# Optimization experiments

Measured on AMD Instinct MI355X. Metric: run time of the kernel, lower is better.

## Reference

```python
import jax, jax.numpy as jnp
import numpy as np
from jax import lax

EMBED = 512
HID = 512
CLASSES = 3
TP, TH, B = 256, 256, 128
IN_DIM = 768


def _gru_cell(x, h, Wih, Whh, bih, bhh):
    # PyTorch GRU cell math. x: [B, in], h: [B, d]
    gi = x @ Wih.T + bih
    gh = h @ Whh.T + bhh
    i_r, i_z, i_n = jnp.split(gi, 3, axis=-1)
    h_r, h_z, h_n = jnp.split(gh, 3, axis=-1)
    r = jax.nn.sigmoid(i_r + h_r)
    z = jax.nn.sigmoid(i_z + h_z)
    n = jnp.tanh(i_n + r * h_n)
    return (1.0 - z) * n + z * h


def _gru_scan(x, h0, Wih, Whh, bih, bhh):
    # x: [T, B, in]; returns outputs [T, B, d]
    def step(h, xt):
        h = _gru_cell(xt, h, Wih, Whh, bih, bhh)
        return h, h
    _, o = lax.scan(step, h0, x)
    return o


def setup_inputs() -> dict:
    key = jax.random.key(0)
    ks = jax.random.split(key, 32)
    s = 0.02
    d = {
        'encoded_p': jax.random.normal(ks[0], (TP, B, IN_DIM), jnp.float32),
        'encoded_h': jax.random.normal(ks[1], (TH, B, IN_DIM), jnp.float32),
        'p_W': jax.random.normal(ks[2], (EMBED, IN_DIM), jnp.float32) * s,
        'p_b': jnp.zeros((EMBED,), jnp.float32),
        'h_W': jax.random.normal(ks[3], (EMBED, IN_DIM), jnp.float32) * s,
        'h_b': jnp.zeros((EMBED,), jnp.float32),
        'pg_Wih': jax.random.normal(ks[4], (3 * HID, EMBED), jnp.float32) * s,
        'pg_Whh': jax.random.normal(ks[5], (3 * HID, HID), jnp.float32) * s,
        'pg_bih': jnp.zeros((3 * HID,), jnp.float32),
        'pg_bhh': jnp.zeros((3 * HID,), jnp.float32),
        'hg_Wih': jax.random.normal(ks[6], (3 * HID, EMBED), jnp.float32) * s,
        'hg_Whh': jax.random.normal(ks[7], (3 * HID, HID), jnp.float32) * s,
        'hg_bih': jnp.zeros((3 * HID,), jnp.float32),
        'hg_bhh': jnp.zeros((3 * HID,), jnp.float32),
        'W_s': jax.random.normal(ks[8], (HID, HID), jnp.float32) * s,
        'W_t': jax.random.normal(ks[9], (HID, HID), jnp.float32) * s,
        'w_e': jax.random.normal(ks[10], (HID, 1), jnp.float32) * s,
        'W_m': jax.random.normal(ks[11], (HID, HID), jnp.float32) * s,
        'm_Wih': jax.random.normal(ks[12], (3 * HID, 2 * HID), jnp.float32) * s,
        'm_Whh': jax.random.normal(ks[13], (3 * HID, HID), jnp.float32) * s,
        'm_bih': jnp.zeros((3 * HID,), jnp.float32),
        'm_bhh': jnp.zeros((3 * HID,), jnp.float32),
        'out_W': jax.random.normal(ks[14], (CLASSES, HID), jnp.float32) * s,
        'out_b': jnp.zeros((CLASSES,), jnp.float32),
        'training': 0,
    }
    return d


def reference(encoded_p, encoded_h, p_W, p_b, h_W, h_b,
              pg_Wih, pg_Whh, pg_bih, pg_bhh,
              hg_Wih, hg_Whh, hg_bih, hg_bhh,
              W_s, W_t, w_e, W_m,
              m_Wih, m_Whh, m_bih, m_bhh,
              out_W, out_b, training):
    batch = encoded_p.shape[1]
    # dropout is identity when training is falsy (reference uses training=0)
    xp = encoded_p @ p_W.T + p_b          # [Tp, B, embed]
    xh = encoded_h @ h_W.T + h_b          # [Th, B, embed]
    h0 = jnp.ones((batch, HID), xp.dtype)  # torch.ones init hidden
    o_p = _gru_scan(xp, h0, pg_Wih, pg_Whh, pg_bih, pg_bhh)  # [Tp, B, d]
    o_h = _gru_scan(xh, h0, hg_Wih, hg_Whh, hg_bih, hg_bhh)  # [Th, B, d]

    Whs = jnp.einsum('tbd,de->tbe', o_p, W_s)  # precompute, fixed across steps
    we = w_e[:, 0]

    def step(h_m, h_t):
        Wht = h_t @ W_t                        # [B, d]
        Wm = h_m @ W_m                         # [B, d]
        M = jnp.tanh(Whs + (Wht + Wm)[None])   # [Tp, B, d]
        logits = jnp.einsum('tbd,d->bt', M, we)  # [B, Tp]
        alpha = jax.nn.softmax(logits, axis=1)
        a_t = jnp.einsum('bt,tbd->bd', alpha, o_p)
        m_t = jnp.concatenate([a_t, h_t], axis=-1)  # [B, 2d]
        h_m = _gru_cell(m_t, h_m, m_Wih, m_Whh, m_bih, m_bhh)
        return h_m, alpha

    h_m0 = jnp.ones((batch, HID), xp.dtype)
    h_star, _alphas = lax.scan(step, h_m0, o_h)
    out = h_star @ out_W.T + out_b
    out = jax.nn.relu(out)  # LAST_NON_LINEAR = True
    return out
```

## Files before the change

kernel.cpp:

```cpp
#include <hip/hip_runtime.h>
#include <cstddef>

#define TSEQ 256
#define NB   128
#define HID  512
#define G3   1536
#define INDIM 768
#define CH   16
#define NWG  256
#define FLS  32

typedef unsigned short bfraw;
using short8 = __attribute__((ext_vector_type(8))) short;
using f32x4  = __attribute__((ext_vector_type(4))) float;

#define MFMA16 __builtin_amdgcn_mfma_f32_16x16x32_bf16

__device__ __forceinline__ float bf2f(unsigned int u){ return __uint_as_float(u<<16); }
__device__ __forceinline__ bfraw f2bf(float f){
  unsigned int u = __float_as_uint(f);
  u += 0x7fffu + ((u>>16)&1u);
  return (bfraw)(u>>16);
}
__device__ __forceinline__ float fsig(float x){
  return __builtin_amdgcn_rcpf(1.0f + __expf(-x));
}
__device__ __forceinline__ float ftanh(float x){
  return 1.0f - 2.0f*__builtin_amdgcn_rcpf(1.0f + __expf(2.0f*x));
}
__device__ __forceinline__ float4 bpf4(const void* p){
  unsigned long long a = __hip_atomic_load((const unsigned long long*)p,     __ATOMIC_RELAXED, __HIP_MEMORY_SCOPE_AGENT);
  unsigned long long b = __hip_atomic_load((const unsigned long long*)p + 1, __ATOMIC_RELAXED, __HIP_MEMORY_SCOPE_AGENT);
  union{ unsigned long long q[2]; float4 f; } cv; cv.q[0]=a; cv.q[1]=b; return cv.f;
}

__device__ __forceinline__ void spin_ge(unsigned* p, unsigned epoch){
  int sp = 0;
  while (__hip_atomic_load(p, __ATOMIC_RELAXED, __HIP_MEMORY_SCOPE_AGENT) < epoch){
    if (sp < 3){ __builtin_amdgcn_s_sleep(1); ++sp; }
    else        __builtin_amdgcn_s_sleep(16);
  }
}

__device__ __forceinline__ void pollN(unsigned* flags, int n, unsigned epoch){
  const int tid = threadIdx.x;
  if (tid < n) spin_ge(&flags[tid*FLS], epoch);
  __syncthreads();
  if (tid == 0)
    (void)__hip_atomic_load(&flags[0], __ATOMIC_ACQUIRE, __HIP_MEMORY_SCOPE_AGENT);
  __syncthreads();
}
__device__ __forceinline__ void setflag(unsigned* f, unsigned v){
  if (threadIdx.x == 0)
    __hip_atomic_store(f, v, __ATOMIC_RELEASE, __HIP_MEMORY_SCOPE_AGENT);
}

__global__ void init_k(unsigned* bar){
  int i = blockIdx.x*256 + threadIdx.x;
  if (i < 4*NWG*FLS) bar[i] = 0u;
}

__global__ void hminit_k(float* hmbuf, bfraw* hm_bf){
  int i = blockIdx.x*256 + threadIdx.x;
  hmbuf[i] = 1.0f;
  hm_bf[i] = (bfraw)0x3f80;
}

__global__ __launch_bounds__(256)
void tconv_k(const float* __restrict__ in, bfraw* __restrict__ out, int R, int Cc){
  __shared__ float t[32][33];
  int c0 = blockIdx.x*32, r0 = blockIdx.y*32;
  int tx = threadIdx.x&31, ty = threadIdx.x>>5;
  #pragma unroll
  for (int i=0;i<32;i+=8) t[ty+i][tx] = in[(size_t)(r0+ty+i)*Cc + c0+tx];
  __syncthreads();
  #pragma unroll
  for (int i=0;i<32;i+=8) out[(size_t)(c0+ty+i)*R + r0+tx] = f2bf(t[tx][ty+i]);
}

__global__ void cvt_k(const float* __restrict__ in, bfraw* __restrict__ out, int n){
  int i = (blockIdx.x*256 + threadIdx.x)*4;
  if (i >= n) return;
  float4 v = *(const float4*)(in+i);
  uint2 o;
  o.x = (unsigned)f2bf(v.x) | ((unsigned)f2bf(v.y)<<16);
  o.y = (unsigned)f2bf(v.z) | ((unsigned)f2bf(v.w)<<16);
  *(uint2*)(out+i) = o;
}

__global__ void wcat_k(const float* __restrict__ mWih, const float* __restrict__ mWhh,
                       bfraw* __restrict__ Wcat){
  size_t gid = (size_t)blockIdx.x*256 + threadIdx.x;
  int np = (int)(gid / 384);
  int k4 = ((int)(gid % 384))*4;
  int dd = np>>2, g = np&3;
  float v[4];
  #pragma unroll
  for (int j=0;j<4;++j){
    int k = k4+j; float x = 0.f;
    if (g==0)      x = (k<1024) ? mWih[(size_t)dd*1024 + k]        : mWhh[(size_t)dd*512 + (k-1024)];
    else if (g==1) x = (k<1024) ? mWih[(size_t)(512+dd)*1024 + k]  : mWhh[(size_t)(512+dd)*512 + (k-1024)];
    else if (g==2) x = (k<1024) ? mWih[(size_t)(1024+dd)*1024 + k] : 0.f;
    else           x = (k<1024) ? 0.f : mWhh[(size_t)(1024+dd)*512 + (k-1024)];
    v[j] = x;
  }
  uint2 o;
  o.x = (unsigned)f2bf(v[0]) | ((unsigned)f2bf(v[1])<<16);
  o.y = (unsigned)f2bf(v[2]) | ((unsigned)f2bf(v[3])<<16);
  *(uint2*)(Wcat + (size_t)np*1536 + k4) = o;
}

__global__ void bpack_k(const float* __restrict__ mbih, const float* __restrict__ mbhh,
                        float* __restrict__ bc){
  int dd = blockIdx.x*256 + threadIdx.x;
  if (dd >= 512) return;
  bc[dd]      = mbih[dd] + mbhh[dd];
  bc[512+dd]  = mbih[512+dd] + mbhh[512+dd];
  bc[1024+dd] = mbih[1024+dd];
  bc[1536+dd] = mbhh[1024+dd];
}

__global__ void fuse_bias_k(const float* __restrict__ Wih, const float* __restrict__ bih,
                            const float* __restrict__ pb, float* __restrict__ bout)
{
  int g = blockIdx.x*256 + threadIdx.x;
  if (g >= G3) return;
  float acc = bih[g];
  const float* w = Wih + (size_t)g*HID;
  for (int e=0;e<HID;e+=4){
    float4 wv = *(const float4*)(w+e);
    float4 pv = *(const float4*)(pb+e);
    acc += wv.x*pv.x + wv.y*pv.y + wv.z*pv.z + wv.w*pv.w;
  }
  bout[g] = acc;
}

template<typename TA, typename TC, bool BIAS>
__global__ __launch_bounds__(256)
void mgemm(const TA* __restrict__ A0, const TA* __restrict__ A1,
           const bfraw* __restrict__ B0, const bfraw* __restrict__ B1,
           const float* __restrict__ bias0, const float* __restrict__ bias1,
           TC* __restrict__ C0, TC* __restrict__ C1,
           int K, int lda, int ldb, int ldc)
{
  const TA* A = blockIdx.z ? A1 : A0;
  const bfraw* B = blockIdx.z ? B1 : B0;
  const float* bias = blockIdx.z ? bias1 : bias0;
  TC* C = blockIdx.z ? C1 : C0;
  __shared__ bfraw Al[128*40];
  __shared__ bfraw Bl[128*40];
  const int tid = threadIdx.x;
  const size_t m0 = (size_t)blockIdx.y*128, n0 = (size_t)blockIdx.x*128;
  const int w = tid>>6, l = tid&63;
  const int wr = (w>>1)*64, wc = (w&1)*64;
  const int fr = l&15, fg = l>>4;
  f32x4 acc[4][4];
  #pragma unroll
  for (int i=0;i<4;++i)
    #pragma unroll
    for (int j=0;j<4;++j) acc[i][j] = (f32x4){0.f,0.f,0.f,0.f};

  const int srow = tid>>1, skc = (tid&1)*16;
  for (int k0=0; k0<K; k0+=32){
    if constexpr (sizeof(TA)==4){
      const float* ap = (const float*)A + (m0+srow)*lda + k0 + skc;
      float4 v0=*(const float4*)ap, v1=*(const float4*)(ap+4),
             v2=*(const float4*)(ap+8), v3=*(const float4*)(ap+12);
      uint4 w0, w1;
      w0.x=(unsigned)f2bf(v0.x)|((unsigned)f2bf(v0.y)<<16);
      w0.y=(unsigned)f2bf(v0.z)|((unsigned)f2bf(v0.w)<<16);
      w0.z=(unsigned)f2bf(v1.x)|((unsigned)f2bf(v1.y)<<16);
      w0.w=(unsigned)f2bf(v1.z)|((unsigned)f2bf(v1.w)<<16);
      w1.x=(unsigned)f2bf(v2.x)|((unsigned)f2bf(v2.y)<<16);
      w1.y=(unsigned)f2bf(v2.z)|((unsigned)f2bf(v2.w)<<16);
      w1.z=(unsigned)f2bf(v3.x)|((unsigned)f2bf(v3.y)<<16);
      w1.w=(unsigned)f2bf(v3.z)|((unsigned)f2bf(v3.w)<<16);
      *(uint4*)&Al[srow*40+skc]   = w0;
      *(uint4*)&Al[srow*40+skc+8] = w1;
    } else {
      const bfraw* ap = (const bfraw*)A + (m0+srow)*lda + k0 + skc;
      *(uint4*)&Al[srow*40+skc]   = *(const uint4*)ap;
      *(uint4*)&Al[srow*40+skc+8] = *(const uint4*)(ap+8);
    }
    {
      const bfraw* bp = B + (n0+srow)*ldb + k0 + skc;
      *(uint4*)&Bl[srow*40+skc]   = *(const uint4*)bp;
      *(uint4*)&Bl[srow*40+skc+8] = *(const uint4*)(bp+8);
    }
    __syncthreads();
    short8 af[4], bfr[4];
    #pragma unroll
    for (int i=0;i<4;++i) af[i]  = *(const short8*)&Al[(wr+i*16+fr)*40 + fg*8];
    #pragma unroll
    for (int j=0;j<4;++j) bfr[j] = *(const short8*)&Bl[(wc+j*16+fr)*40 + fg*8];
    #pragma unroll
    for (int i=0;i<4;++i)
      #pragma unroll
      for (int j=0;j<4;++j)
        acc[i][j] = MFMA16(af[i], bfr[j], acc[i][j], 0,0,0);
    __syncthreads();
  }
  #pragma unroll
  for (int i=0;i<4;++i){
    #pragma unroll
    for (int j=0;j<4;++j){
      size_t n = n0 + wc + j*16 + fr;
      float bv = BIAS ? bias[n] : 0.f;
      #pragma unroll
      for (int r=0;r<4;++r){
        size_t m = m0 + wr + i*16 + fg*4 + r;
        float v = acc[i][j][r] + bv;
        if constexpr (sizeof(TC)==2) ((bfraw*)C)[m*ldc + n] = f2bf(v);
        else                         ((float*)C)[m*ldc + n] = v;
      }
    }
  }
}

__global__ __launch_bounds__(512, 2)
void scanB(const float* __restrict__ GIp, const float* __restrict__ GIh,
           const bfraw* __restrict__ Whhp, const bfraw* __restrict__ Whhh,
           const float* __restrict__ bhhp, const float* __restrict__ bhhh,
           float* __restrict__ hst, bfraw* __restrict__ o_p, bfraw* __restrict__ o_h,
           int c0, unsigned* __restrict__ bar)
{
  extern __shared__ char smem[];
  bfraw* wl = (bfraw*)smem;
  float* sh = (float*)(smem + 98304);
  const int wg = blockIdx.x;
  const int z = wg>>7, rem = wg&127;
  const int bg = rem>>4, dg = rem&15;
  const float* GI  = z ? GIh : GIp;
  const bfraw* Wb  = z ? Whhh : Whhp;
  const float* bhh = z ? bhhh : bhhp;
  bfraw* ob = z ? o_h : o_p;
  float* hz = hst + (size_t)z*2*NB*HID;
  const int tid = threadIdx.x;
  unsigned* bfl = bar + 3*NWG*FLS;
  unsigned* grp = bfl + (size_t)(z*128 + bg*16)*FLS;
  unsigned* own = bfl + (size_t)wg*FLS;

  #pragma unroll
  for (int g=0; g<3; ++g){
    const unsigned* src = (const unsigned*)(Wb + (size_t)(g*512 + dg*32)*512);
    for (int j=0; j<16; ++j){
      int iu = tid + j*512;
      unsigned v = src[iu];
      int d = iu>>8, kk = (iu&255)*2;
      int idx0 = g*16384 + (kk>>2)*128 + d*4 + (kk&3);
      *((unsigned*)wl + (idx0>>1)) = v;
    }
  }
  __syncthreads();

  const int bl = tid>>5, dl = tid&31;
  const int d = dg*32+dl, bglob = bg*16+bl;
  const float br = bhh[d], bz = bhh[512+d], bn = bhh[1024+d];

  #pragma clang loop unroll(disable)
  for (int tt=0; tt<CH; ++tt){
    const int t = c0+tt;
    if (t > 0) pollN(grp, 16, (unsigned)t);
    if (t == 0){
      for (int j=0;j<4;++j){
        int i4 = tid + j*512;
        *(float4*)&sh[i4*4] = (float4){1.f,1.f,1.f,1.f};
      }
    } else {
      const float* hp = hz + (size_t)((t-1)&1)*NB*HID + (size_t)bg*16*HID;
      for (int j=0;j<4;++j){
        int i4 = tid + j*512;
        *(float4*)&sh[i4*4] = *(const float4*)&hp[i4*4];
      }
    }
    __syncthreads();
    float ar = br, az = bz, an = bn;
    const float* hb = sh + bl*512;
    for (int k=0;k<512;k+=4){
      float4 h4 = *(const float4*)(hb+k);
      int base = (k>>2)*128 + dl*4;
      uint2 wr = *(const uint2*)(wl + base);
      uint2 wz = *(const uint2*)(wl + 16384 + base);
      uint2 wn = *(const uint2*)(wl + 32768 + base);
      ar += h4.x*bf2f(wr.x&0xffffu) + h4.y*bf2f(wr.x>>16) + h4.z*bf2f(wr.y&0xffffu) + h4.w*bf2f(wr.y>>16);
      az += h4.x*bf2f(wz.x&0xffffu) + h4.y*bf2f(wz.x>>16) + h4.z*bf2f(wz.y&0xffffu) + h4.w*bf2f(wz.y>>16);
      an += h4.x*bf2f(wn.x&0xffffu) + h4.y*bf2f(wn.x>>16) + h4.z*bf2f(wn.y&0xffffu) + h4.w*bf2f(wn.y>>16);
    }
    const float* gi = GI + ((size_t)tt*NB + bglob)*G3;
    float r  = fsig(gi[d] + ar);
    float zz = fsig(gi[512+d] + az);
    float n  = ftanh(gi[1024+d] + r*an);
    float hp = hb[d];
    float hv = (1.0f-zz)*n + zz*hp;
    (hz + (size_t)(t&1)*NB*HID)[(size_t)bglob*HID + d] = hv;
    ob[((size_t)t*NB + bglob)*HID + d] = f2bf(hv);
    __syncthreads();
    setflag(own, (unsigned)(t+1));
  }
}

__global__ __launch_bounds__(512, 2)
void scanD(const bfraw* __restrict__ Whs, const bfraw* __restrict__ o_p,
           const bfraw* __restrict__ o_h,
           const bfraw* __restrict__ WtT, const bfraw* __restrict__ WmT,
           const float* __restrict__ w_e,
           const bfraw* __restrict__ Wcat, const float* __restrict__ bc,
           float* __restrict__ hmbuf, bfraw* __restrict__ hm_bf,
           bfraw* __restrict__ a_bf, float* __restrict__ Lbuf, float* __restrict__ Gx,
           const float* __restrict__ outW, const float* __restrict__ outb,
           float* __restrict__ out, unsigned* __restrict__ bar)
{
  extern __shared__ char smem[];
  bfraw* whs_l = (bfraw*)smem;
  float* pt    = (float*)(smem + 131072);
  float* xlf   = (float*)(smem + 147456);
  float* hml   = (float*)(smem + 149504);
  float* c_l   = (float*)(smem + 151552);
  float* lp0   = (float*)(smem + 152576);
  float* lp1   = (float*)(smem + 153600);
  float* l_s   = (float*)(smem + 154624);
  float* red   = (float*)(smem + 155648);

  const int wg = blockIdx.x, tid = threadIdx.x;
  const int b = wg>>1, dh = wg&1;
  unsigned* pf  = bar;
  unsigned* afl = bar + NWG*FLS;
  unsigned* hfl = bar + 2*NWG*FLS;

  for (int it=0; it<16; ++it){
    int idx = tid + it*512;
    int tq = idx>>5, c = idx&31;
    const bfraw* src = Whs + ((size_t)tq*NB + b)*HID + dh*256 + c*8;
    *(uint4*)&whs_l[tq*256 + ((c ^ (tq&15))<<3)] = *(const uint4*)src;
  }
  const int cc_ = tid&31;
  float we8[8];
  #pragma unroll
  for (int r=0;r<8;++r) we8[r] = w_e[dh*256 + cc_*8 + r];
  __syncthreads();

  const int gw = tid>>6, gl = tid&63, gfr = gl&15, gfg = gl>>4;
  const int m0w = gw*16;
  const int n0g = (wg&127)*16;
  const bfraw* wrowA = Wcat + (size_t)(n0g+gfr)*1536;

  #pragma clang loop unroll(disable)
  for (int t=0; t<TSEQ; ++t){
    const int rs = (t+1)&1;
    const bfraw* hmr = hm_bf + (size_t)rs*65536;
    const float* hpr = hmbuf + (size_t)rs*65536;
    bfraw* hmw = hm_bf + (size_t)(t&1)*65536;
    float* hpw = hmbuf + (size_t)(t&1)*65536;

    if (t > 0) pollN(hfl, 128, (unsigned)t);

    if (tid < 64){
      uint4 u = *(const uint4*)(o_h + ((size_t)t*NB + b)*HID + tid*8);
      float4 f0, f1;
      f0.x=bf2f(u.x&0xffffu); f0.y=bf2f(u.x>>16); f0.z=bf2f(u.y&0xffffu); f0.w=bf2f(u.y>>16);
      f1.x=bf2f(u.z&0xffffu); f1.y=bf2f(u.z>>16); f1.z=bf2f(u.w&0xffffu); f1.w=bf2f(u.w>>16);
      *(float4*)&xlf[tid*8]   = f0;
      *(float4*)&xlf[tid*8+4] = f1;
    } else if (tid < 192){
      int i2 = tid - 64;
      *(float4*)&hml[i2*4] = *(const float4*)(hpr + (size_t)b*HID + i2*4);
    }
    __syncthreads();

    {
      const int el = tid>>1, kh = tid&1;
      const bfraw* wt = WtT + (size_t)(dh*256+el)*HID + kh*256;
      const bfraw* wm = WmT + (size_t)(dh*256+el)*HID + kh*256;
      const float* xv = xlf + kh*256;
      const float* hv = hml + kh*256;
      float acc = 0.f;
      #pragma unroll 4
      for (int k8=0;k8<32;++k8){
        uint4 wu = *(const uint4*)(wt+k8*8);
        uint4 mu = *(const uint4*)(wm+k8*8);
        float4 x0 = *(const float4*)(xv+k8*8), x1 = *(const float4*)(xv+k8*8+4);
        float4 h0 = *(const float4*)(hv+k8*8), h1 = *(const float4*)(hv+k8*8+4);
        acc += x0.x*bf2f(wu.x&0xffffu) + x0.y*bf2f(wu.x>>16) + x0.z*bf2f(wu.y&0xffffu) + x0.w*bf2f(wu.y>>16);
        acc += x1.x*bf2f(wu.z&0xffffu) + x1.y*bf2f(wu.z>>16) + x1.z*bf2f(wu.w&0xffffu) + x1.w*bf2f(wu.w>>16);
        acc += h0.x*bf2f(mu.x&0xffffu) + h0.y*bf2f(mu.x>>16) + h0.z*bf2f(mu.y&0xffffu) + h0.w*bf2f(mu.y>>16);
        acc += h1.x*bf2f(mu.z&0xffffu) + h1.y*bf2f(mu.z>>16) + h1.z*bf2f(mu.w&0xffffu) + h1.w*bf2f(mu.w>>16);
      }
      acc += __shfl_xor(acc, 1);
      if (kh == 0) c_l[el] = acc;
    }
    __syncthreads();

    {
      const int tqs = tid>>5;
      float c8[8];
      *(float4*)&c8[0] = *(const float4*)&c_l[cc_*8];
      *(float4*)&c8[4] = *(const float4*)&c_l[cc_*8+4];
      #pragma unroll 2
      for (int i=0;i<16;++i){
        int tq = tqs + i*16;
        uint4 u = *(const uint4*)&whs_l[tq*256 + ((cc_ ^ (tq&15))<<3)];
        float s = 0.f;
        #pragma unroll
        for (int j=0;j<4;++j){
          unsigned uu = ((const unsigned*)&u)[j];
          s += ftanh(bf2f(uu&0xffffu) + c8[j*2])   * we8[j*2];
          s += ftanh(bf2f(uu>>16)     + c8[j*2+1]) * we8[j*2+1];
        }
        #pragma unroll
        for (int off=16; off; off>>=1) s += __shfl_xor(s, off);
        if (cc_ == 0) lp0[tq] = s;
      }
    }
    __syncthreads();
    if (tid < 64) *(float4*)&Lbuf[(size_t)wg*256 + tid*4] = *(const float4*)&lp0[tid*4];
    __syncthreads();
    setflag(&pf[wg*FLS], (unsigned)(t+1));

    const int dgrp = tid&31, tqs2 = tid>>5, d8 = dgrp*8;
    const bfraw* opb = o_p + (size_t)b*HID + dh*256 + d8;
    uint4 uu[16];
    #pragma unroll
    for (int i=0;i<16;++i)
      uu[i] = *(const uint4*)(opb + (size_t)(tqs2*16 + i)*NB*HID);

    f32x4 accA = {0.f,0.f,0.f,0.f};
    if (wg < 128){
      const bfraw* hrow = hmr + (size_t)(m0w+gfr)*HID;
      #pragma unroll
      for (int kk=0; kk<16; ++kk){
        short8 af = *(const short8*)(hrow + kk*32 + gfg*8);
        short8 bv = *(const short8*)(wrowA + 1024 + kk*32 + gfg*8);
        accA = MFMA16(af, bv, accA, 0,0,0);
      }
    } else {
      f32x4 accB = {0.f,0.f,0.f,0.f};
      const bfraw* xrow = o_h + ((size_t)t*NB + m0w+gfr)*HID;
      #pragma unroll
      for (int kk=0; kk<16; ++kk){
        short8 af = *(const short8*)(xrow + kk*32 + gfg*8);
        short8 bv = *(const short8*)(wrowA + 512 + kk*32 + gfg*8);
        accB = MFMA16(af, bv, accB, 0,0,0);
      }
      #pragma unroll
      for (int rr=0; rr<4; ++rr)
        Gx[(size_t)(m0w + gfg*4 + rr)*2048 + n0g + gfr] = accB[rr];
    }

    if (tid == 0) spin_ge(&pf[(wg^1)*FLS], (unsigned)(t+1));
    __syncthreads();
    if (tid < 64) *(float4*)&lp1[tid*4] = bpf4(&Lbuf[(size_t)(wg^1)*256 + tid*4]);
    __syncthreads();

    {
      const int lane = tid&63;
      float v = -1e30f, e = 0.f;
      if (tid < TSEQ){
        v = lp0[tid] + lp1[tid];
        float m = v;
        #pragma unroll
        for (int off=32; off; off>>=1) m = fmaxf(m, __shfl_xor(m, off));
        if (lane==0) red[tid>>6] = m;
      }
      __syncthreads();
      float mx = fmaxf(fmaxf(red[0],red[1]), fmaxf(red[2],red[3]));
      if (tid < TSEQ){
        e = __expf(v - mx);
        float s2 = e;
        #pragma unroll
        for (int off=32; off; off>>=1) s2 += __shfl_xor(s2, off);
        if (lane==0) red[8+(tid>>6)] = s2;
      }
      __syncthreads();
      float S = red[8]+red[9]+red[10]+red[11];
      if (tid < TSEQ) l_s[tid] = e * __builtin_amdgcn_rcpf(S);
      __syncthreads();
    }

    {
      float a0=0,a1=0,a2=0,a3=0,a4=0,a5=0,a6=0,a7=0;
      #pragma unroll
      for (int i=0;i<16;++i){
        float al = l_s[tqs2*16 + i];
        uint4 u = uu[i];
        a0 += al*bf2f(u.x&0xffffu); a1 += al*bf2f(u.x>>16);
        a2 += al*bf2f(u.y&0xffffu); a3 += al*bf2f(u.y>>16);
        a4 += al*bf2f(u.z&0xffffu); a5 += al*bf2f(u.z>>16);
        a6 += al*bf2f(u.w&0xffffu); a7 += al*bf2f(u.w>>16);
      }
      *(float4*)&pt[tqs2*256+d8]   = (float4){a0,a1,a2,a3};
      *(float4*)&pt[tqs2*256+d8+4] = (float4){a4,a5,a6,a7};
      __syncthreads();
      if (tid < 256){
        float sA = 0.f;
        #pragma unroll
        for (int ss=0;ss<16;++ss) sA += pt[ss*256 + tid];
        float sB = __shfl_down(sA, 1);
        if ((tid&1)==0){
          unsigned pk = (unsigned)f2bf(sA) | ((unsigned)f2bf(sB)<<16);
          *(unsigned*)(a_bf + (size_t)b*HID + dh*256 + tid) = pk;
        }
      }
    }
    __syncthreads();
    setflag(&afl[wg*FLS], (unsigned)(t+1));

    if (wg < 128){
      pollN(afl, 256, (unsigned)(t+1));
      const bfraw* arow = a_bf + (size_t)(m0w+gfr)*HID;
      #pragma unroll
      for (int kk=0; kk<16; ++kk){
        short8 af = *(const short8*)(arow + kk*32 + gfg*8);
        short8 bv = *(const short8*)(wrowA + kk*32 + gfg*8);
        accA = MFMA16(af, bv, accA, 0,0,0);
      }
      const int np = n0g + gfr, dd = np>>2, g = np&3;
      #pragma unroll
      for (int rr=0; rr<4; ++rr){
        float x0 = accA[rr] + Gx[(size_t)(m0w + gfg*4 + rr)*2048 + np];
        float x1 = __shfl_xor(x0, 1);
        float x2 = __shfl_xor(x0, 2);
        float x3 = __shfl_xor(x1, 2);
        if (g==0){
          int b3 = m0w + gfg*4 + rr;
          float hp = hpr[(size_t)b3*HID + dd];
          float rg = fsig(x0 + bc[dd]);
          float zg = fsig(x1 + bc[512+dd]);
          float gn = ftanh(x2 + bc[1024+dd] + rg*(x3 + bc[1536+dd]));
          float h = (1.f-zg)*gn + zg*hp;
          hpw[(size_t)b3*HID + dd] = h;
          hmw[(size_t)b3*HID + dd] = f2bf(h);
        }
      }
      __syncthreads();
      setflag(&hfl[wg*FLS], (unsigned)(t+1));
    }
  }

  if (wg == 0){
    pollN(hfl, 128, (unsigned)TSEQ);
    if (tid < NB*3){
      const float* hf = hmbuf + (size_t)((TSEQ-1)&1)*65536;
      int b2 = tid/3, c = tid%3;
      float acc = outb[c];
      const float* h = hf + (size_t)b2*HID;
      const float* w = outW + (size_t)c*HID;
      for (int d2=0; d2<HID; ++d2) acc = fmaf(h[d2], w[d2], acc);
      out[tid] = fmaxf(acc, 0.f);
    }
  }
}

extern "C" void kernel_launch(void* const* d_in, const int* in_sizes, int n_in,
                              void* d_out, int out_size, void* d_ws, size_t ws_size,
                              hipStream_t stream)
{
  const float* Ep    = (const float*)d_in[0];
  const float* Eh    = (const float*)d_in[1];
  const float* p_W   = (const float*)d_in[2];
  const float* p_b   = (const float*)d_in[3];
  const float* h_W   = (const float*)d_in[4];
  const float* h_b   = (const float*)d_in[5];
  const float* pgWih = (const float*)d_in[6];
  const float* pgWhh = (const float*)d_in[7];
  const float* pgbih = (const float*)d_in[8];
  const float* pgbhh = (const float*)d_in[9];
  const float* hgWih = (const float*)d_in[10];
  const float* hgWhh = (const float*)d_in[11];
  const float* hgbih = (const float*)d_in[12];
  const float* hgbhh = (const float*)d_in[13];
  const float* W_s   = (const float*)d_in[14];
  const float* W_t   = (const float*)d_in[15];
  const float* w_e   = (const float*)d_in[16];
  const float* W_m   = (const float*)d_in[17];
  const float* mWih  = (const float*)d_in[18];
  const float* mWhh  = (const float*)d_in[19];
  const float* mbih  = (const float*)d_in[20];
  const float* mbhh  = (const float*)d_in[21];
  const float* outW  = (const float*)d_in[22];
  const float* outb  = (const float*)d_in[23];

  const size_t OB    = (size_t)TSEQ*NB*HID*sizeof(bfraw);
  const size_t RB    = OB;
  const size_t WFB   = (size_t)G3*INDIM*sizeof(bfraw);
  const size_t SQB   = (size_t)HID*HID*sizeof(bfraw);
  const size_t WHHB  = (size_t)G3*HID*sizeof(bfraw);
  const size_t WCATB = (size_t)2048*1536*sizeof(bfraw);
  const size_t BARB  = (size_t)4*NWG*FLS*sizeof(unsigned);
  const size_t needed = 2*OB + RB + 2*WFB + 3*SQB + 2*WHHB + WCATB
                        + 8192 + 2*6144
                        + 4*262144 + 2*262144 + 2*131072
                        + BARB;
  if (ws_size < needed) return;

  char* p = (char*)d_ws;
  bfraw* o_p_bf = (bfraw*)p; p += OB;
  bfraw* o_h_bf = (bfraw*)p; p += OB;
  char*  Rreg   = p;         p += RB;
  bfraw* Wfp_bf = (bfraw*)p; p += WFB;
  bfraw* Wfh_bf = (bfraw*)p; p += WFB;
  bfraw* WsT_bf = (bfraw*)p; p += SQB;
  bfraw* WtT_bf = (bfraw*)p; p += SQB;
  bfraw* WmT_bf = (bfraw*)p; p += SQB;
  bfraw* Whhp_bf= (bfraw*)p; p += WHHB;
  bfraw* Whhh_bf= (bfraw*)p; p += WHHB;
  bfraw* Wcat_bf= (bfraw*)p; p += WCATB;
  float* bc     = (float*)p; p += 8192;
  float* bfp    = (float*)p; p += 6144;
  float* bfh    = (float*)p; p += 6144;
  float* hst    = (float*)p; p += 4*262144;
  float* hmbuf  = (float*)p; p += 2*262144;
  bfraw* hm_bf  = (bfraw*)p; p += 2*131072;
  unsigned* bar = (unsigned*)p; p += BARB;

  bfraw* pWT_bf = (bfraw*)Rreg;
  bfraw* hWT_bf = (bfraw*)(Rreg + (size_t)INDIM*HID*sizeof(bfraw));
  float* GIp_c  = (float*)Rreg;
  float* GIh_c  = (float*)(Rreg + (size_t)CH*NB*G3*sizeof(float));
  bfraw* Whs_bf = (bfraw*)Rreg;
  float* Lbuf   = (float*)Wfp_bf;
  bfraw* a_bf   = (bfraw*)((char*)Wfp_bf + 2097152);
  float* Gx     = (float*)((char*)Wfp_bf + WFB);

  (void)hipFuncSetAttribute((const void*)scanB, hipFuncAttributeMaxDynamicSharedMemorySize, 131072);
  (void)hipFuncSetAttribute((const void*)scanD, hipFuncAttributeMaxDynamicSharedMemorySize, 155776);

  dim3 b256(256), b512(512);

  init_k<<<dim3(128), b256, 0, stream>>>(bar);
  hminit_k<<<dim3(512), b256, 0, stream>>>(hmbuf, hm_bf);

  tconv_k<<<dim3(INDIM/32, HID/32), b256, 0, stream>>>(p_W, pWT_bf, HID, INDIM);
  tconv_k<<<dim3(INDIM/32, HID/32), b256, 0, stream>>>(h_W, hWT_bf, HID, INDIM);
  tconv_k<<<dim3(HID/32, HID/32),  b256, 0, stream>>>(W_s, WsT_bf, HID, HID);
  tconv_k<<<dim3(HID/32, HID/32),  b256, 0, stream>>>(W_t, WtT_bf, HID, HID);
  tconv_k<<<dim3(HID/32, HID/32),  b256, 0, stream>>>(W_m, WmT_bf, HID, HID);
  cvt_k<<<dim3((G3*HID)/1024), b256, 0, stream>>>(pgWhh, Whhp_bf, G3*HID);
  cvt_k<<<dim3((G3*HID)/1024), b256, 0, stream>>>(hgWhh, Whhh_bf, G3*HID);
  wcat_k<<<dim3(3072), b256, 0, stream>>>(mWih, mWhh, Wcat_bf);
  bpack_k<<<dim3(2), b256, 0, stream>>>(mbih, mbhh, bc);
  fuse_bias_k<<<dim3(G3/256), b256, 0, stream>>>(pgWih, pgbih, p_b, bfp);
  fuse_bias_k<<<dim3(G3/256), b256, 0, stream>>>(hgWih, hgbih, h_b, bfh);
  mgemm<float, bfraw, false><<<dim3(INDIM/128, G3/128, 2), b256, 0, stream>>>(
    pgWih, hgWih, pWT_bf, hWT_bf, nullptr, nullptr, Wfp_bf, Wfh_bf,
    HID, HID, HID, INDIM);

  for (int c = 0; c < TSEQ/CH; ++c){
    mgemm<float, float, true><<<dim3(G3/128, (CH*NB)/128, 2), b256, 0, stream>>>(
      Ep + (size_t)c*CH*NB*INDIM, Eh + (size_t)c*CH*NB*INDIM,
      Wfp_bf, Wfh_bf, bfp, bfh, GIp_c, GIh_c,
      INDIM, INDIM, INDIM, G3);
    scanB<<<dim3(NWG), b512, 131072, stream>>>(
      GIp_c, GIh_c, Whhp_bf, Whhh_bf, pgbhh, hgbhh,
      hst, o_p_bf, o_h_bf, c*CH, bar);
  }

  mgemm<bfraw, bfraw, false><<<dim3(HID/128, (TSEQ*NB)/128, 1), b256, 0, stream>>>(
    o_p_bf, o_p_bf, WsT_bf, WsT_bf, nullptr, nullptr, Whs_bf, Whs_bf,
    HID, HID, HID, HID);

  scanD<<<dim3(NWG), b512, 155776, stream>>>(
    Whs_bf, o_p_bf, o_h_bf, WtT_bf, WmT_bf, w_e, Wcat_bf, bc,
    hmbuf, hm_bf, a_bf, Lbuf, Gx,
    outW, outb, (float*)d_out, bar);
}
```

Baseline: 22.15 ms.

## Retile GRU GEMM by batch groups to replace global barriers with targeted flag waits

The mem-GRU output tiling changes from each workgroup covering a 16-column slice across all batch rows to each covering a 16-row batch group by a 128-column slice. With this, each workgroup only depends on the attention outputs and hidden-state flags of the workgroups producing its batch rows. The full 128/256-flag polls become waits on a small subset of flags followed by an acquire load. This cuts global synchronization latency in the sequential loop, but the dependency bookkeeping must be exact or memory ordering could break.

```diff
diff --git a/kernel.cpp b/kernel.cpp
--- a/kernel.cpp
+++ b/kernel.cpp
@@ -339,10 +339,11 @@
   for (int r=0;r<8;++r) we8[r] = w_e[dh*256 + cc_*8 + r];
   __syncthreads();
 
+  const int gs = wg&127, gbgrp = gs>>4, gddg = gs&15;
   const int gw = tid>>6, gl = tid&63, gfr = gl&15, gfg = gl>>4;
-  const int m0w = gw*16;
-  const int n0g = (wg&127)*16;
-  const bfraw* wrowA = Wcat + (size_t)(n0g+gfr)*1536;
+  const int n0w = gddg*128 + gw*16;
+  const int mb0 = gbgrp*16;
+  const bfraw* wrowA = Wcat + (size_t)(n0w+gfr)*1536;
 
   #pragma clang loop unroll(disable)
   for (int t=0; t<TSEQ; ++t){
@@ -352,7 +353,15 @@
     bfraw* hmw = hm_bf + (size_t)(t&1)*65536;
     float* hpw = hmbuf + (size_t)(t&1)*65536;
 
-    if (t > 0) pollN(hfl, 128, (unsigned)t);
+    if (t > 0){
+      if (tid < 16) spin_ge(&hfl[((b>>4)*16 + tid)*FLS], (unsigned)t);
+      else if (wg < 128 && tid < 32) spin_ge(&hfl[(gbgrp*16 + (tid-16))*FLS], (unsigned)t);
+      else if (wg >= 128 && tid == 16) spin_ge(&hfl[gs*FLS], (unsigned)t);
+      __syncthreads();
+      if (tid == 0)
+        (void)__hip_atomic_load(&hfl[0], __ATOMIC_ACQUIRE, __HIP_MEMORY_SCOPE_AGENT);
+      __syncthreads();
+    }
 
     if (tid < 64){
       uint4 u = *(const uint4*)(o_h + ((size_t)t*NB + b)*HID + tid*8);
@@ -425,7 +434,7 @@
 
     f32x4 accA = {0.f,0.f,0.f,0.f};
     if (wg < 128){
-      const bfraw* hrow = hmr + (size_t)(m0w+gfr)*HID;
+      const bfraw* hrow = hmr + (size_t)(mb0+gfr)*HID;
       #pragma unroll
       for (int kk=0; kk<16; ++kk){
         short8 af = *(const short8*)(hrow + kk*32 + gfg*8);
@@ -434,7 +443,7 @@
       }
     } else {
       f32x4 accB = {0.f,0.f,0.f,0.f};
-      const bfraw* xrow = o_h + ((size_t)t*NB + m0w+gfr)*HID;
+      const bfraw* xrow = o_h + ((size_t)t*NB + mb0+gfr)*HID;
       #pragma unroll
       for (int kk=0; kk<16; ++kk){
         short8 af = *(const short8*)(xrow + kk*32 + gfg*8);
@@ -443,7 +452,7 @@
       }
       #pragma unroll
       for (int rr=0; rr<4; ++rr)
-        Gx[(size_t)(m0w + gfg*4 + rr)*2048 + n0g + gfr] = accB[rr];
+        Gx[(size_t)(mb0 + gfg*4 + rr)*2048 + n0w + gfr] = accB[rr];
     }
 
     if (tid == 0) spin_ge(&pf[(wg^1)*FLS], (unsigned)(t+1));
@@ -505,23 +514,29 @@
     setflag(&afl[wg*FLS], (unsigned)(t+1));
 
     if (wg < 128){
-      pollN(afl, 256, (unsigned)(t+1));
-      const bfraw* arow = a_bf + (size_t)(m0w+gfr)*HID;
+      if (tid < 32) spin_ge(&afl[(gbgrp*32 + tid)*FLS], (unsigned)(t+1));
+      else if (tid == 32) spin_ge(&afl[(128 + gs)*FLS], (unsigned)(t+1));
+      __syncthreads();
+      if (tid == 0)
+        (void)__hip_atomic_load(&afl[0], __ATOMIC_ACQUIRE, __HIP_MEMORY_SCOPE_AGENT);
+      __syncthreads();
+
+      const bfraw* arow = a_bf + (size_t)(mb0+gfr)*HID;
       #pragma unroll
       for (int kk=0; kk<16; ++kk){
         short8 af = *(const short8*)(arow + kk*32 + gfg*8);
         short8 bv = *(const short8*)(wrowA + kk*32 + gfg*8);
         accA = MFMA16(af, bv, accA, 0,0,0);
       }
-      const int np = n0g + gfr, dd = np>>2, g = np&3;
+      const int np = n0w + gfr, dd = np>>2, g = np&3;
       #pragma unroll
       for (int rr=0; rr<4; ++rr){
-        float x0 = accA[rr] + Gx[(size_t)(m0w + gfg*4 + rr)*2048 + np];
+        float x0 = accA[rr] + Gx[(size_t)(mb0 + gfg*4 + rr)*2048 + np];
         float x1 = __shfl_xor(x0, 1);
         float x2 = __shfl_xor(x0, 2);
         float x3 = __shfl_xor(x1, 2);
         if (g==0){
-          int b3 = m0w + gfg*4 + rr;
+          int b3 = mb0 + gfg*4 + rr;
           float hp = hpr[(size_t)b3*HID + dd];
           float rg = fsig(x0 + bc[dd]);
           float zg = fsig(x1 + bc[512+dd]);
```

New measurement: 20.77 ms. 1.07x faster.
